# Kernel optimization log

Measured on AMD Instinct MI355X. Metric: run time of the kernel, lower is better.

## Reference

```python
import jax, jax.numpy as jnp
import numpy as np

V = 100000
E = 1600000
BN_EPS = 1e-5


def spmm(edge_index, vals, X):
    # X: (V, Cin, B); sparse L @ X via scatter-add. y[r] += w * X[c]
    rows, cols = edge_index[0], edge_index[1]
    return jnp.zeros_like(X).at[rows].add(vals[:, None, None] * X[cols])


def cheb_conv(x, edge_index, vals, w, b=None):
    # x: (B, Cin, V), w: (K, Cin, Cout) -> (B, Cout, V)
    K = w.shape[0]
    x0 = jnp.transpose(x, (2, 1, 0))  # (V, Cin, B)
    xs = [x0]
    if K > 1:
        x1 = spmm(edge_index, vals, x0)
        xs.append(x1)
        for _ in range(2, K):
            x2 = 2.0 * spmm(edge_index, vals, x1) - x0
            xs.append(x2)
            x0, x1 = x1, x2
    xk = jnp.stack(xs)  # (K, V, Cin, B)
    out = jnp.einsum('kvcb,kco->bov', xk, w)
    if b is not None:
        out = out + b[None, :, None]
    return out


def batch_norm(x, g, b):
    # training-mode BatchNorm1d on (B, C, V): stats over (B, V), biased var
    m = jnp.mean(x, axis=(0, 2), keepdims=True)
    v = jnp.var(x, axis=(0, 2), keepdims=True)
    return g[None, :, None] * (x - m) * jax.lax.rsqrt(v + BN_EPS) + b[None, :, None]


def setup_inputs() -> dict:
    key = jax.random.key(0)
    ks = jax.random.split(key, 8)
    x = jax.random.normal(ks[0], (4, 32, V), dtype=jnp.float32)
    edge_index = jax.random.randint(ks[1], (2, E), 0, V, dtype=jnp.int32)
    # small values keep the K=4 Chebyshev recursion well-scaled
    lap_vals = 0.1 * jax.random.normal(ks[2], (E,), dtype=jnp.float32)
    def w(k, K, cin, cout):
        s = 1.0 / np.sqrt(K * cin)
        return s * jax.random.normal(k, (K, cin, cout), dtype=jnp.float32)
    return {
        'x': x, 'edge_index': edge_index, 'lap_vals': lap_vals,
        'in_bn_g': jnp.ones((32,), jnp.float32), 'in_bn_b': jnp.zeros((32,), jnp.float32),
        'in_w': w(ks[3], 4, 32, 64), 'in_b': jnp.zeros((64,), jnp.float32),
        'h0_bn_g': jnp.ones((64,), jnp.float32), 'h0_bn_b': jnp.zeros((64,), jnp.float32),
        'h0_w': w(ks[4], 4, 64, 64), 'h0_b': jnp.zeros((64,), jnp.float32),
        'h1_bn_g': jnp.ones((64,), jnp.float32), 'h1_bn_b': jnp.zeros((64,), jnp.float32),
        'h1_w': w(ks[5], 4, 64, 32), 'h1_b': jnp.zeros((32,), jnp.float32),
    }


def reference(x, edge_index, lap_vals, in_bn_g, in_bn_b, in_w, in_b,
              h0_bn_g, h0_bn_b, h0_w, h0_b, h1_bn_g, h1_bn_b, h1_w, h1_b):
    xn = batch_norm(x, in_bn_g, in_bn_b)
    out = cheb_conv(xn, edge_index, lap_vals, in_w, in_b)
    # hidden layer 0
    out = jax.nn.relu(out)
    out = batch_norm(out, h0_bn_g, h0_bn_b)
    out = cheb_conv(out, edge_index, lap_vals, h0_w, h0_b)
    # hidden layer 1
    out = jax.nn.relu(out)
    out = batch_norm(out, h1_bn_g, h1_bn_b)
    out = cheb_conv(out, edge_index, lap_vals, h1_w, h1_b)
    # in_channels == out_channels -> Identity shortcut on the BN'ed input
    return jax.nn.relu(out + xn)
```

## Files before the change

kernel.cpp:

```cpp
#include <hip/hip_runtime.h>
#include <cstdint>
#include <cstddef>

#define VN 100000
#define EN 1600000
static constexpr float BN_EPS_F = 1e-5f;
static constexpr float INV_N = 1.0f / 400000.0f;

using short8 = __attribute__((ext_vector_type(8))) short;
using f32x4  = __attribute__((ext_vector_type(4))) float;

__device__ __forceinline__ float bf_lo(unsigned int p) {
  return __builtin_bit_cast(float, p << 16);
}
__device__ __forceinline__ float bf_hi(unsigned int p) {
  return __builtin_bit_cast(float, p & 0xffff0000u);
}
__device__ __forceinline__ float bf1(unsigned short u) {
  return __builtin_bit_cast(float, ((unsigned int)u) << 16);
}
__device__ __forceinline__ unsigned short f2bf(float f) {
  unsigned int x = __builtin_bit_cast(unsigned int, f);
  x += 0x7fffu + ((x >> 16) & 1u);
  return (unsigned short)(x >> 16);
}
__device__ __forceinline__ unsigned int pack2(float a, float b) {
  return (unsigned int)f2bf(a) | ((unsigned int)f2bf(b) << 16);
}

__global__ __launch_bounds__(256) void stats_x_kernel(const float* __restrict__ x,
                                                      float* __restrict__ stats) {
  const int p = blockIdx.x & 127;
  const int chunk = blockIdx.x >> 7;
  const int c = p & 31, b = p >> 5;
  const float* base = x + ((size_t)b * 32 + c) * VN + chunk * 12500;
  float s = 0.f, s2 = 0.f;
  for (int i = threadIdx.x; i < 12500; i += 256) {
    float v = base[i];
    s += v; s2 += v * v;
  }
  __shared__ float r1[256], r2[256];
  r1[threadIdx.x] = s; r2[threadIdx.x] = s2;
  __syncthreads();
  for (int off = 128; off > 0; off >>= 1) {
    if (threadIdx.x < off) {
      r1[threadIdx.x] += r1[threadIdx.x + off];
      r2[threadIdx.x] += r2[threadIdx.x + off];
    }
    __syncthreads();
  }
  if (threadIdx.x == 0) {
    atomicAdd(&stats[c], r1[0]);
    atomicAdd(&stats[64 + c], r2[0]);
  }
}

__global__ void finalize_stats_kernel(float* __restrict__ stats,
                                      const float* __restrict__ g,
                                      const float* __restrict__ beta, int C) {
  int c = threadIdx.x;
  if (c < C) {
    float m = stats[c] * INV_N;
    float var = stats[64 + c] * INV_N - m * m;
    float sc = g[c] * rsqrtf(var + BN_EPS_F);
    stats[128 + c] = sc;
    stats[192 + c] = beta[c] - m * sc;
  }
}

__global__ __launch_bounds__(128) void bn_transpose_kernel(const float* __restrict__ x,
                                                           const float* __restrict__ stats,
                                                           unsigned short* __restrict__ xn) {
  const int tid = threadIdx.x;
  const int b = tid >> 5, c = tid & 31;
  const int v0 = blockIdx.x * 64;
  const float sc = stats[128 + c], sh = stats[192 + c];
  const float* src = x + ((size_t)b * 32 + c) * VN;
  for (int i = 0; i < 64; i++) {
    int v = v0 + i;
    if (v < VN) xn[(size_t)v * 128 + tid] = f2bf(sc * src[v] + sh);
  }
}

__global__ __launch_bounds__(256) void pack_wb_kernel(const float* __restrict__ W,
                                                      unsigned short* __restrict__ Wb,
                                                      int Cin, int Cout) {
  const int i = blockIdx.x * 256 + threadIdx.x;
  const int KC = Cin >> 5, T = Cout >> 4;
  const int tot = 4 * KC * T * 512;
  if (i >= tot) return;
  const int j = i & 7;
  const int l = (i >> 3) & 63;
  const int rem = i >> 9;
  const int t = rem % T;
  const int kc = (rem / T) % KC;
  const int k = rem / (T * KC);
  const int c = kc * 32 + (l >> 4) * 8 + j;
  const int o = t * 16 + (l & 15);
  Wb[i] = f2bf(W[((size_t)k * Cin + c) * Cout + o]);
}

__global__ __launch_bounds__(256) void hist_kernel(const int* __restrict__ rows,
                                                   int* __restrict__ cnt) {
  int i = blockIdx.x * blockDim.x + threadIdx.x;
  const int stride = gridDim.x * blockDim.x;
  for (; i < EN; i += stride) atomicAdd(&cnt[rows[i]], 1);
}

__global__ __launch_bounds__(256) void scan1_kernel(const int* __restrict__ cnt,
                                                    int* __restrict__ rp,
                                                    int* __restrict__ chunkSums) {
  __shared__ int sh[256];
  const int t = threadIdx.x;
  const int base = blockIdx.x * 2048 + t * 8;
  int vals[8]; int tot = 0;
#pragma unroll
  for (int i = 0; i < 8; i++) {
    int idx = base + i;
    int v = (idx < VN) ? cnt[idx] : 0;
    vals[i] = v; tot += v;
  }
  sh[t] = tot;
  __syncthreads();
  for (int off = 1; off < 256; off <<= 1) {
    int v = (t >= off) ? sh[t - off] : 0;
    __syncthreads();
    sh[t] += v;
    __syncthreads();
  }
  int run = sh[t] - tot;
#pragma unroll
  for (int i = 0; i < 8; i++) {
    int idx = base + i;
    if (idx < VN) rp[idx] = run;
    run += vals[i];
  }
  if (t == 255) chunkSums[blockIdx.x] = sh[255];
}

__global__ void scan2_kernel(const int* __restrict__ chunkSums,
                             int* __restrict__ chunkOff,
                             int* __restrict__ rp, int nChunks) {
  if (threadIdx.x == 0 && blockIdx.x == 0) {
    int off = 0;
    for (int j = 0; j < nChunks; j++) { chunkOff[j] = off; off += chunkSums[j]; }
    rp[VN] = off;
  }
}

__global__ __launch_bounds__(256) void scan3_kernel(int* __restrict__ rp,
                                                    const int* __restrict__ chunkOff,
                                                    int* __restrict__ fill) {
  int i = blockIdx.x * 256 + threadIdx.x;
  if (i < VN) {
    int v = rp[i] + chunkOff[i >> 11];
    rp[i] = v;
    fill[i] = v;
  }
}

__global__ __launch_bounds__(256) void fill_kernel(const int* __restrict__ rows,
                                                   const int* __restrict__ cols,
                                                   const float* __restrict__ lap,
                                                   int* __restrict__ fill,
                                                   int* __restrict__ cols_s,
                                                   float* __restrict__ vals_s) {
  int i = blockIdx.x * blockDim.x + threadIdx.x;
  const int stride = gridDim.x * blockDim.x;
  for (; i < EN; i += stride) {
    int r = rows[i];
    int pos = atomicAdd(&fill[r], 1);
    cols_s[pos] = cols[i];
    vals_s[pos] = lap[i];
  }
}

template <int EPL, int MODE>
__global__ __launch_bounds__(256, 8) void spmm_kernel(const int* __restrict__ rp,
                                                   const int* __restrict__ cs,
                                                   const float* __restrict__ vs,
                                                   const unsigned short* __restrict__ X, int XS,
                                                   const unsigned short* __restrict__ P, int PS,
                                                   const unsigned short* __restrict__ Q, int QS,
                                                   unsigned short* __restrict__ Y, int YS) {
  const int lane = threadIdx.x & 63;
  const int row = blockIdx.x * 4 + (threadIdx.x >> 6);
  const int start = rp[row], end = rp[row + 1];
  float acc[EPL];
#pragma unroll
  for (int j = 0; j < EPL; j++) acc[j] = 0.f;
  int e = start;
  for (; e + 4 <= end; e += 4) {
    const int c0 = cs[e], c1 = cs[e + 1], c2 = cs[e + 2], c3 = cs[e + 3];
    const float w0 = vs[e], w1 = vs[e + 1], w2 = vs[e + 2], w3 = vs[e + 3];
    if constexpr (EPL == 4) {
      const uint2 q0 = *reinterpret_cast<const uint2*>(X + (size_t)c0 * XS + lane * 4);
      const uint2 q1 = *reinterpret_cast<const uint2*>(X + (size_t)c1 * XS + lane * 4);
      const uint2 q2 = *reinterpret_cast<const uint2*>(X + (size_t)c2 * XS + lane * 4);
      const uint2 q3 = *reinterpret_cast<const uint2*>(X + (size_t)c3 * XS + lane * 4);
      acc[0] += w0 * bf_lo(q0.x) + w1 * bf_lo(q1.x) + w2 * bf_lo(q2.x) + w3 * bf_lo(q3.x);
      acc[1] += w0 * bf_hi(q0.x) + w1 * bf_hi(q1.x) + w2 * bf_hi(q2.x) + w3 * bf_hi(q3.x);
      acc[2] += w0 * bf_lo(q0.y) + w1 * bf_lo(q1.y) + w2 * bf_lo(q2.y) + w3 * bf_lo(q3.y);
      acc[3] += w0 * bf_hi(q0.y) + w1 * bf_hi(q1.y) + w2 * bf_hi(q2.y) + w3 * bf_hi(q3.y);
    } else {
      const unsigned int q0 = *reinterpret_cast<const unsigned int*>(X + (size_t)c0 * XS + lane * 2);
      const unsigned int q1 = *reinterpret_cast<const unsigned int*>(X + (size_t)c1 * XS + lane * 2);
      const unsigned int q2 = *reinterpret_cast<const unsigned int*>(X + (size_t)c2 * XS + lane * 2);
      const unsigned int q3 = *reinterpret_cast<const unsigned int*>(X + (size_t)c3 * XS + lane * 2);
      acc[0] += w0 * bf_lo(q0) + w1 * bf_lo(q1) + w2 * bf_lo(q2) + w3 * bf_lo(q3);
      acc[1] += w0 * bf_hi(q0) + w1 * bf_hi(q1) + w2 * bf_hi(q2) + w3 * bf_hi(q3);
    }
  }
  for (; e < end; e++) {
    const int c0 = cs[e];
    const float w0 = vs[e];
    if constexpr (EPL == 4) {
      const uint2 q0 = *reinterpret_cast<const uint2*>(X + (size_t)c0 * XS + lane * 4);
      acc[0] += w0 * bf_lo(q0.x);
      acc[1] += w0 * bf_hi(q0.x);
      acc[2] += w0 * bf_lo(q0.y);
      acc[3] += w0 * bf_hi(q0.y);
    } else {
      const unsigned int q0 = *reinterpret_cast<const unsigned int*>(X + (size_t)c0 * XS + lane * 2);
      acc[0] += w0 * bf_lo(q0);
      acc[1] += w0 * bf_hi(q0);
    }
  }
  if constexpr (EPL == 4) {
    float r0 = acc[0], r1 = acc[1], r2 = acc[2], r3 = acc[3];
    if constexpr (MODE == 1) {
      const uint2 p = *reinterpret_cast<const uint2*>(P + (size_t)row * PS + lane * 4);
      r0 = 2.f * r0 - bf_lo(p.x);
      r1 = 2.f * r1 - bf_hi(p.x);
      r2 = 2.f * r2 - bf_lo(p.y);
      r3 = 2.f * r3 - bf_hi(p.y);
    }
    uint2 r;
    r.x = pack2(r0, r1);
    r.y = pack2(r2, r3);
    *reinterpret_cast<uint2*>(Y + (size_t)row * YS + lane * 4) = r;
  } else {
    float r0 = acc[0], r1 = acc[1];
    if constexpr (MODE == 1) {
      const unsigned int p = *reinterpret_cast<const unsigned int*>(P + (size_t)row * PS + lane * 2);
      r0 = 2.f * r0 - bf_lo(p);
      r1 = 2.f * r1 - bf_hi(p);
    } else if constexpr (MODE == 2) {
      const unsigned int p = *reinterpret_cast<const unsigned int*>(P + (size_t)row * PS + lane * 2);
      r0 = 2.f * r0 + bf_lo(p);
      r1 = 2.f * r1 + bf_hi(p);
    } else if constexpr (MODE == 3) {
      const unsigned int p = *reinterpret_cast<const unsigned int*>(P + (size_t)row * PS + lane * 2);
      const unsigned int qq = *reinterpret_cast<const unsigned int*>(Q + (size_t)row * QS + lane * 2);
      r0 = 2.f * r0 - bf_lo(qq) + bf_lo(p);
      r1 = 2.f * r1 - bf_hi(qq) + bf_hi(p);
    } else if constexpr (MODE == 4) {
      const unsigned int p = *reinterpret_cast<const unsigned int*>(P + (size_t)row * PS + lane * 2);
      const unsigned int qq = *reinterpret_cast<const unsigned int*>(Q + (size_t)row * QS + lane * 2);
      r0 = r0 - bf_lo(qq) + bf_lo(p);
      r1 = r1 - bf_hi(qq) + bf_hi(p);
    }
    *reinterpret_cast<unsigned int*>(Y + (size_t)row * YS + lane * 2) = pack2(r0, r1);
  }
}

template <int Cin, int Cout, int X0S>
__global__ __launch_bounds__(256, 8) void fused_cheb_kernel(const int* __restrict__ rp,
                                                         const int* __restrict__ cs,
                                                         const float* __restrict__ vs,
                                                         const unsigned short* __restrict__ X0,
                                                         unsigned short* __restrict__ A,
                                                         const unsigned short* __restrict__ B,
                                                         const unsigned short* __restrict__ Wb,
                                                         const float* __restrict__ Bias) {
  constexpr int EPL = Cin * 4 / 64;
  constexpr int ROWSH = Cin * 4;
  __shared__ unsigned short t3s[4 * ROWSH];
  const int lane = threadIdx.x & 63;
  const int wv = threadIdx.x >> 6;
  const int row0 = blockIdx.x * 4;
  const int row = row0 + wv;

  float g[EPL];
#pragma unroll
  for (int j = 0; j < EPL; j++) g[j] = 0.f;
  const int start = rp[row], end = rp[row + 1];
  int e = start;
  for (; e + 4 <= end; e += 4) {
    const int c0 = cs[e], c1 = cs[e + 1], c2 = cs[e + 2], c3 = cs[e + 3];
    const float w0 = vs[e], w1 = vs[e + 1], w2 = vs[e + 2], w3 = vs[e + 3];
    if constexpr (EPL == 4) {
      const uint2 q0 = *reinterpret_cast<const uint2*>(B + (size_t)c0 * 256 + lane * 4);
      const uint2 q1 = *reinterpret_cast<const uint2*>(B + (size_t)c1 * 256 + lane * 4);
      const uint2 q2 = *reinterpret_cast<const uint2*>(B + (size_t)c2 * 256 + lane * 4);
      const uint2 q3 = *reinterpret_cast<const uint2*>(B + (size_t)c3 * 256 + lane * 4);
      g[0] += w0 * bf_lo(q0.x) + w1 * bf_lo(q1.x) + w2 * bf_lo(q2.x) + w3 * bf_lo(q3.x);
      g[1] += w0 * bf_hi(q0.x) + w1 * bf_hi(q1.x) + w2 * bf_hi(q2.x) + w3 * bf_hi(q3.x);
      g[2] += w0 * bf_lo(q0.y) + w1 * bf_lo(q1.y) + w2 * bf_lo(q2.y) + w3 * bf_lo(q3.y);
      g[3] += w0 * bf_hi(q0.y) + w1 * bf_hi(q1.y) + w2 * bf_hi(q2.y) + w3 * bf_hi(q3.y);
    } else {
      const unsigned int q0 = *reinterpret_cast<const unsigned int*>(B + (size_t)c0 * 256 + lane * 2);
      const unsigned int q1 = *reinterpret_cast<const unsigned int*>(B + (size_t)c1 * 256 + lane * 2);
      const unsigned int q2 = *reinterpret_cast<const unsigned int*>(B + (size_t)c2 * 256 + lane * 2);
      const unsigned int q3 = *reinterpret_cast<const unsigned int*>(B + (size_t)c3 * 256 + lane * 2);
      g[0] += w0 * bf_lo(q0) + w1 * bf_lo(q1) + w2 * bf_lo(q2) + w3 * bf_lo(q3);
      g[1] += w0 * bf_hi(q0) + w1 * bf_hi(q1) + w2 * bf_hi(q2) + w3 * bf_hi(q3);
    }
  }
  for (; e < end; e++) {
    const int c0 = cs[e];
    const float w0 = vs[e];
    if constexpr (EPL == 4) {
      const uint2 q0 = *reinterpret_cast<const uint2*>(B + (size_t)c0 * 256 + lane * 4);
      g[0] += w0 * bf_lo(q0.x);
      g[1] += w0 * bf_hi(q0.x);
      g[2] += w0 * bf_lo(q0.y);
      g[3] += w0 * bf_hi(q0.y);
    } else {
      const unsigned int q0 = *reinterpret_cast<const unsigned int*>(B + (size_t)c0 * 256 + lane * 2);
      g[0] += w0 * bf_lo(q0);
      g[1] += w0 * bf_hi(q0);
    }
  }
  {
    unsigned int* tw = reinterpret_cast<unsigned int*>(t3s + wv * ROWSH);
    if constexpr (EPL == 4) {
      const uint2 p = *reinterpret_cast<const uint2*>(A + (size_t)row * 256 + lane * 4);
      tw[lane * 2]     = pack2(2.f * g[0] - bf_lo(p.x), 2.f * g[1] - bf_hi(p.x));
      tw[lane * 2 + 1] = pack2(2.f * g[2] - bf_lo(p.y), 2.f * g[3] - bf_hi(p.y));
    } else {
      const unsigned int p = *reinterpret_cast<const unsigned int*>(A + (size_t)row * 256 + lane * 2);
      tw[lane] = pack2(2.f * g[0] - bf_lo(p), 2.f * g[1] - bf_hi(p));
    }
  }
  __syncthreads();

  constexpr int KC = Cin / 32;
  constexpr int T = Cout / 16;
  const int col = lane & 15, quad = lane >> 4;
  const int t = wv % T;
  const int ar = col >> 2, ab = col & 3;

  const unsigned short* xap[3];
  xap[0] = X0 + (size_t)(row0 + ar) * X0S + ab * Cin + quad * 8;
  xap[1] = A  + (size_t)(row0 + ar) * 256 + ab * Cin + quad * 8;
  xap[2] = B  + (size_t)(row0 + ar) * 256 + ab * Cin + quad * 8;
  const unsigned short* wb = Wb + (size_t)t * 512 + lane * 8;

  f32x4 acc = {0.f, 0.f, 0.f, 0.f};
#pragma unroll
  for (int k = 0; k < 3; k++) {
#pragma unroll
    for (int kc = 0; kc < KC; kc++) {
      const short8 af = *reinterpret_cast<const short8*>(xap[k] + kc * 32);
      const short8 bf = *reinterpret_cast<const short8*>(wb + (size_t)(k * KC + kc) * T * 512);
      acc = __builtin_amdgcn_mfma_f32_16x16x32_bf16(af, bf, acc, 0, 0, 0);
    }
  }
#pragma unroll
  for (int kc = 0; kc < KC; kc++) {
    const short8 af = *reinterpret_cast<const short8*>(&t3s[ar * ROWSH + ab * Cin + kc * 32 + quad * 8]);
    const short8 bf = *reinterpret_cast<const short8*>(wb + (size_t)(3 * KC + kc) * T * 512);
    acc = __builtin_amdgcn_mfma_f32_16x16x32_bf16(af, bf, acc, 0, 0, 0);
  }
  __syncthreads();

  if (T == 4 || wv < 2) {
    const int og = t * 16 + col;
    const float bs = Bias[og];
#pragma unroll
    for (int r = 0; r < 4; r++) {
      A[(size_t)(row0 + quad) * 256 + r * Cout + og] = f2bf(acc[r] + bs);
    }
  }
}

__global__ __launch_bounds__(256, 8) void gemm_z_kernel(const unsigned short* __restrict__ XL,
                                                        const unsigned short* __restrict__ Wb,
                                                        const float* __restrict__ Bias,
                                                        unsigned short* __restrict__ Z) {
  const int lane = threadIdx.x & 63;
  const int wv = threadIdx.x >> 6;
  const int row0 = blockIdx.x * 4;
  const int col = lane & 15, quad = lane >> 4;
  const int ar = col >> 2, ab = col & 3;
  const unsigned short* xa = XL + (size_t)(row0 + ar) * 256 + ab * 64 + quad * 8;
  const unsigned short* wb = Wb + (size_t)wv * 4 * 512 + lane * 8;
  unsigned short* zr = Z + (size_t)wv * VN * 128;
#pragma unroll
  for (int t = 0; t < 2; t++) {
    f32x4 acc = {0.f, 0.f, 0.f, 0.f};
#pragma unroll
    for (int kc = 0; kc < 2; kc++) {
      const short8 af = *reinterpret_cast<const short8*>(xa + kc * 32);
      const short8 bf = *reinterpret_cast<const short8*>(wb + (size_t)(kc * 2 + t) * 512);
      acc = __builtin_amdgcn_mfma_f32_16x16x32_bf16(af, bf, acc, 0, 0, 0);
    }
    const int og = t * 16 + col;
    const float bs = (wv == 0) ? Bias[og] : 0.f;
#pragma unroll
    for (int r = 0; r < 4; r++) {
      zr[(size_t)(row0 + quad) * 128 + r * 32 + og] = f2bf(acc[r] + bs);
    }
  }
}

__global__ __launch_bounds__(256) void stats_out_kernel(const unsigned short* __restrict__ SRC,
                                                        float* __restrict__ stats) {
  const int tid = threadIdx.x;
  const int per = (VN + gridDim.x - 1) / gridDim.x;
  const int v0 = blockIdx.x * per;
  const int v1 = (v0 + per < VN) ? (v0 + per) : VN;
  float s = 0.f, s2 = 0.f;
  for (int v = v0; v < v1; v++) {
    float val = bf1(SRC[(size_t)v * 256 + tid]);
    val = fmaxf(val, 0.f);
    s += val; s2 += val * val;
  }
  __shared__ float r1[256], r2[256];
  r1[tid] = s; r2[tid] = s2;
  __syncthreads();
  if (tid < 64) {
    float a = r1[tid] + r1[tid + 64] + r1[tid + 128] + r1[tid + 192];
    float b = r2[tid] + r2[tid + 64] + r2[tid + 128] + r2[tid + 192];
    atomicAdd(&stats[tid], a);
    atomicAdd(&stats[64 + tid], b);
  }
}

__global__ __launch_bounds__(256) void bn_relu_kernel(const unsigned short* __restrict__ SRC,
                                                      const float* __restrict__ stats,
                                                      unsigned short* __restrict__ DST) {
  const int i = blockIdx.x * 256 + threadIdx.x;
  const int w = i & 63;
  const int o0 = (w & 15) * 4;
  const float4 sc4 = *reinterpret_cast<const float4*>(stats + 128 + o0);
  const float4 sh4 = *reinterpret_cast<const float4*>(stats + 192 + o0);
  const uint2 q = reinterpret_cast<const uint2*>(SRC)[i];
  float a = fmaxf(bf_lo(q.x), 0.f);
  float b = fmaxf(bf_hi(q.x), 0.f);
  float c = fmaxf(bf_lo(q.y), 0.f);
  float d = fmaxf(bf_hi(q.y), 0.f);
  uint2 r;
  r.x = pack2(a * sc4.x + sh4.x, b * sc4.y + sh4.y);
  r.y = pack2(c * sc4.z + sh4.z, d * sc4.w + sh4.w);
  reinterpret_cast<uint2*>(DST)[i] = r;
}

__global__ __launch_bounds__(256) void final_kernel(const unsigned short* __restrict__ SRC,
                                                    const unsigned short* __restrict__ xn,
                                                    float* __restrict__ out) {
  const int lane = threadIdx.x & 63;
  const int grp = threadIdx.x >> 6;
  const int v = blockIdx.x * 64 + lane;
  if (v >= VN) return;
  for (int ob = grp; ob < 128; ob += 4) {
    float val = bf1(SRC[(size_t)v * 128 + ob]) + bf1(xn[(size_t)v * 128 + ob]);
    val = fmaxf(val, 0.f);
    out[(size_t)ob * VN + v] = val;
  }
}

static constexpr size_t align_up(size_t x) { return (x + 255) & ~(size_t)255; }
static constexpr size_t OFF_RP    = 0;
static constexpr size_t OFF_FILL  = align_up(OFF_RP + (size_t)(VN + 1) * 4);
static constexpr size_t OFF_CHS   = align_up(OFF_FILL + (size_t)VN * 4);
static constexpr size_t OFF_CHO   = align_up(OFF_CHS + 256);
static constexpr size_t OFF_STATS = align_up(OFF_CHO + 256);
static constexpr size_t OFF_WP    = align_up(OFF_STATS + 1024);
static constexpr size_t OFF_CS    = align_up(OFF_WP + 32768 * 2);
static constexpr size_t OFF_VS    = align_up(OFF_CS + (size_t)EN * 4);
static constexpr size_t OFF_XN    = align_up(OFF_VS + (size_t)EN * 4);
static constexpr size_t OFF_XL    = align_up(OFF_XN + (size_t)VN * 128 * 2);
static constexpr size_t OFF_A     = align_up(OFF_XL + (size_t)VN * 256 * 2);
static constexpr size_t OFF_B     = align_up(OFF_A + (size_t)VN * 256 * 2);
static constexpr size_t OFF_END   = OFF_B + (size_t)VN * 256 * 2;
static_assert(OFF_B == OFF_A + (size_t)VN * 256 * 2, "A|B must be contiguous for Clenshaw z layout");

extern "C" void kernel_launch(void* const* d_in, const int* in_sizes, int n_in,
                              void* d_out, int out_size, void* d_ws, size_t ws_size,
                              hipStream_t stream) {
  if (ws_size < OFF_END) return;

  const float* x       = (const float*)d_in[0];
  const int*   rows    = (const int*)d_in[1];
  const int*   cols    = rows + EN;
  const float* lap     = (const float*)d_in[2];
  const float* in_bn_g = (const float*)d_in[3];
  const float* in_bn_b = (const float*)d_in[4];
  const float* in_w    = (const float*)d_in[5];
  const float* in_b    = (const float*)d_in[6];
  const float* h0_bn_g = (const float*)d_in[7];
  const float* h0_bn_b = (const float*)d_in[8];
  const float* h0_w    = (const float*)d_in[9];
  const float* h0_b    = (const float*)d_in[10];
  const float* h1_bn_g = (const float*)d_in[11];
  const float* h1_bn_b = (const float*)d_in[12];
  const float* h1_w    = (const float*)d_in[13];
  const float* h1_b    = (const float*)d_in[14];
  float* outp = (float*)d_out;

  char* ws = (char*)d_ws;
  int*   rp     = (int*)(ws + OFF_RP);
  int*   fill   = (int*)(ws + OFF_FILL);
  int*   chS    = (int*)(ws + OFF_CHS);
  int*   chO    = (int*)(ws + OFF_CHO);
  float* stats  = (float*)(ws + OFF_STATS);
  unsigned short* wbIn = (unsigned short*)(ws + OFF_WP);
  unsigned short* wbH0 = wbIn + 8192;
  unsigned short* wbH1 = wbH0 + 16384;
  int*   cs     = (int*)(ws + OFF_CS);
  float* vs     = (float*)(ws + OFF_VS);
  unsigned short* xn = (unsigned short*)(ws + OFF_XN);
  unsigned short* XL = (unsigned short*)(ws + OFF_XL);
  unsigned short* A  = (unsigned short*)(ws + OFF_A);
  unsigned short* B  = (unsigned short*)(ws + OFF_B);

  const int nChunks = (VN + 2047) / 2048;

  pack_wb_kernel<<<32, 256, 0, stream>>>(in_w, wbIn, 32, 64);
  pack_wb_kernel<<<64, 256, 0, stream>>>(h0_w, wbH0, 64, 64);
  pack_wb_kernel<<<32, 256, 0, stream>>>(h1_w, wbH1, 64, 32);

  hipMemsetAsync(stats, 0, 1024, stream);
  stats_x_kernel<<<1024, 256, 0, stream>>>(x, stats);
  finalize_stats_kernel<<<1, 64, 0, stream>>>(stats, in_bn_g, in_bn_b, 32);
  bn_transpose_kernel<<<1563, 128, 0, stream>>>(x, stats, xn);

  hipMemsetAsync(fill, 0, (size_t)VN * 4, stream);
  hist_kernel<<<2048, 256, 0, stream>>>(rows, fill);
  scan1_kernel<<<nChunks, 256, 0, stream>>>(fill, rp, chS);
  scan2_kernel<<<1, 64, 0, stream>>>(chS, chO, rp, nChunks);
  scan3_kernel<<<(VN + 255) / 256, 256, 0, stream>>>(rp, chO, fill);
  fill_kernel<<<2048, 256, 0, stream>>>(rows, cols, lap, fill, cs, vs);

  spmm_kernel<2, 0><<<VN / 4, 256, 0, stream>>>(rp, cs, vs, xn, 128, nullptr, 0, nullptr, 0, A, 256);
  spmm_kernel<2, 1><<<VN / 4, 256, 0, stream>>>(rp, cs, vs, A, 256, xn, 128, nullptr, 0, B, 256);
  fused_cheb_kernel<32, 64, 128><<<VN / 4, 256, 0, stream>>>(rp, cs, vs, xn, A, B, wbIn, in_b);
  hipMemsetAsync(stats, 0, 1024, stream);
  stats_out_kernel<<<256, 256, 0, stream>>>(A, stats);
  finalize_stats_kernel<<<1, 64, 0, stream>>>(stats, h0_bn_g, h0_bn_b, 64);
  bn_relu_kernel<<<VN * 64 / 256, 256, 0, stream>>>(A, stats, XL);

  spmm_kernel<4, 0><<<VN / 4, 256, 0, stream>>>(rp, cs, vs, XL, 256, nullptr, 0, nullptr, 0, A, 256);
  spmm_kernel<4, 1><<<VN / 4, 256, 0, stream>>>(rp, cs, vs, A, 256, XL, 256, nullptr, 0, B, 256);
  fused_cheb_kernel<64, 64, 256><<<VN / 4, 256, 0, stream>>>(rp, cs, vs, XL, A, B, wbH0, h0_b);
  hipMemsetAsync(stats, 0, 1024, stream);
  stats_out_kernel<<<256, 256, 0, stream>>>(A, stats);
  finalize_stats_kernel<<<1, 64, 0, stream>>>(stats, h1_bn_g, h1_bn_b, 64);
  bn_relu_kernel<<<VN * 64 / 256, 256, 0, stream>>>(A, stats, XL);

  {
    unsigned short* Z  = A;
    unsigned short* z0 = Z;
    unsigned short* z1 = Z + (size_t)VN * 128;
    unsigned short* z2 = Z + (size_t)VN * 256;
    unsigned short* z3 = Z + (size_t)VN * 384;
    gemm_z_kernel<<<VN / 4, 256, 0, stream>>>(XL, wbH1, h1_b, Z);
    spmm_kernel<2, 2><<<VN / 4, 256, 0, stream>>>(rp, cs, vs, z3, 128, z2, 128, nullptr, 0, z2, 128);
    spmm_kernel<2, 3><<<VN / 4, 256, 0, stream>>>(rp, cs, vs, z2, 128, z1, 128, z3, 128, z1, 128);
    spmm_kernel<2, 4><<<VN / 4, 256, 0, stream>>>(rp, cs, vs, z1, 128, z0, 128, z2, 128, z0, 128);
    final_kernel<<<1563, 256, 0, stream>>>(z0, xn, outp);
  }
}
```

Baseline: 1.637 ms.

## Fuse BN+ReLU into SpMM gathers and GEMM loads, unroll gathers by eight

Removes the standalone bn_relu kernels. The BatchNorm scale/shift and ReLU are now applied on the fly wherever the pre-activation buffer is read: the SpMM gather (AX), the recurrence term (AP), the fused Chebyshev GEMM A-operand (AFF0) and the Clenshaw gemm_z input. The gather loop is factored into a shared helper unrolled by eight, so more loads are in flight. Buffers are remapped so that layer-0 intermediates use a 128-stride layout. This saves a full read and write of the activations per layer, at the cost of recomputing the affine and ReLU for every gathered neighbour (about 16 per row).

```diff
diff --git a/kernel.cpp b/kernel.cpp
--- a/kernel.cpp
+++ b/kernel.cpp
@@ -26,6 +26,101 @@
 }
 __device__ __forceinline__ unsigned int pack2(float a, float b) {
   return (unsigned int)f2bf(a) | ((unsigned int)f2bf(b) << 16);
+}
+
+template <int EPL, bool AX>
+__device__ __forceinline__ void gather_accum(int start, int end,
+    const int* __restrict__ cs, const float* __restrict__ vs,
+    const unsigned short* __restrict__ X, int XS, int lane,
+    float4 sc, float4 sh, float* acc) {
+  int e = start;
+  if constexpr (EPL == 4) {
+    for (; e + 8 <= end; e += 8) {
+      uint2 q[8]; float w[8];
+#pragma unroll
+      for (int u = 0; u < 8; u++) {
+        q[u] = *reinterpret_cast<const uint2*>(X + (size_t)cs[e + u] * XS + lane * 4);
+        w[u] = vs[e + u];
+      }
+#pragma unroll
+      for (int u = 0; u < 8; u++) {
+        float v0 = bf_lo(q[u].x), v1 = bf_hi(q[u].x), v2 = bf_lo(q[u].y), v3 = bf_hi(q[u].y);
+        if constexpr (AX) {
+          v0 = fmaxf(v0, 0.f) * sc.x + sh.x;
+          v1 = fmaxf(v1, 0.f) * sc.y + sh.y;
+          v2 = fmaxf(v2, 0.f) * sc.z + sh.z;
+          v3 = fmaxf(v3, 0.f) * sc.w + sh.w;
+        }
+        acc[0] += w[u] * v0; acc[1] += w[u] * v1;
+        acc[2] += w[u] * v2; acc[3] += w[u] * v3;
+      }
+    }
+    for (; e + 4 <= end; e += 4) {
+      uint2 q[4]; float w[4];
+#pragma unroll
+      for (int u = 0; u < 4; u++) {
+        q[u] = *reinterpret_cast<const uint2*>(X + (size_t)cs[e + u] * XS + lane * 4);
+        w[u] = vs[e + u];
+      }
+#pragma unroll
+      for (int u = 0; u < 4; u++) {
+        float v0 = bf_lo(q[u].x), v1 = bf_hi(q[u].x), v2 = bf_lo(q[u].y), v3 = bf_hi(q[u].y);
+        if constexpr (AX) {
+          v0 = fmaxf(v0, 0.f) * sc.x + sh.x;
+          v1 = fmaxf(v1, 0.f) * sc.y + sh.y;
+          v2 = fmaxf(v2, 0.f) * sc.z + sh.z;
+          v3 = fmaxf(v3, 0.f) * sc.w + sh.w;
+        }
+        acc[0] += w[u] * v0; acc[1] += w[u] * v1;
+        acc[2] += w[u] * v2; acc[3] += w[u] * v3;
+      }
+    }
+    for (; e < end; e++) {
+      const uint2 q = *reinterpret_cast<const uint2*>(X + (size_t)cs[e] * XS + lane * 4);
+      const float w = vs[e];
+      float v0 = bf_lo(q.x), v1 = bf_hi(q.x), v2 = bf_lo(q.y), v3 = bf_hi(q.y);
+      if constexpr (AX) {
+        v0 = fmaxf(v0, 0.f) * sc.x + sh.x;
+        v1 = fmaxf(v1, 0.f) * sc.y + sh.y;
+        v2 = fmaxf(v2, 0.f) * sc.z + sh.z;
+        v3 = fmaxf(v3, 0.f) * sc.w + sh.w;
+      }
+      acc[0] += w * v0; acc[1] += w * v1; acc[2] += w * v2; acc[3] += w * v3;
+    }
+  } else {
+    for (; e + 8 <= end; e += 8) {
+      unsigned int q[8]; float w[8];
+#pragma unroll
+      for (int u = 0; u < 8; u++) {
+        q[u] = *reinterpret_cast<const unsigned int*>(X + (size_t)cs[e + u] * XS + lane * 2);
+        w[u] = vs[e + u];
+      }
+#pragma unroll
+      for (int u = 0; u < 8; u++) {
+        acc[0] += w[u] * bf_lo(q[u]);
+        acc[1] += w[u] * bf_hi(q[u]);
+      }
+    }
+    for (; e + 4 <= end; e += 4) {
+      unsigned int q[4]; float w[4];
+#pragma unroll
+      for (int u = 0; u < 4; u++) {
+        q[u] = *reinterpret_cast<const unsigned int*>(X + (size_t)cs[e + u] * XS + lane * 2);
+        w[u] = vs[e + u];
+      }
+#pragma unroll
+      for (int u = 0; u < 4; u++) {
+        acc[0] += w[u] * bf_lo(q[u]);
+        acc[1] += w[u] * bf_hi(q[u]);
+      }
+    }
+    for (; e < end; e++) {
+      const unsigned int q = *reinterpret_cast<const unsigned int*>(X + (size_t)cs[e] * XS + lane * 2);
+      const float w = vs[e];
+      acc[0] += w * bf_lo(q);
+      acc[1] += w * bf_hi(q);
+    }
+  }
 }
 
 __global__ __launch_bounds__(256) void stats_x_kernel(const float* __restrict__ x,
@@ -175,65 +270,44 @@
   }
 }
 
-template <int EPL, int MODE>
+template <int EPL, int MODE, bool AX, bool AP>
 __global__ __launch_bounds__(256, 8) void spmm_kernel(const int* __restrict__ rp,
                                                    const int* __restrict__ cs,
                                                    const float* __restrict__ vs,
                                                    const unsigned short* __restrict__ X, int XS,
                                                    const unsigned short* __restrict__ P, int PS,
                                                    const unsigned short* __restrict__ Q, int QS,
-                                                   unsigned short* __restrict__ Y, int YS) {
+                                                   unsigned short* __restrict__ Y, int YS,
+                                                   const float* __restrict__ bnp) {
   const int lane = threadIdx.x & 63;
   const int row = blockIdx.x * 4 + (threadIdx.x >> 6);
   const int start = rp[row], end = rp[row + 1];
+  float4 sc = {0.f, 0.f, 0.f, 0.f}, sh = {0.f, 0.f, 0.f, 0.f};
+  if constexpr (AX || AP) {
+    const int c0 = (lane * 4) & 63;
+    sc = *reinterpret_cast<const float4*>(bnp + c0);
+    sh = *reinterpret_cast<const float4*>(bnp + 64 + c0);
+  }
   float acc[EPL];
 #pragma unroll
   for (int j = 0; j < EPL; j++) acc[j] = 0.f;
-  int e = start;
-  for (; e + 4 <= end; e += 4) {
-    const int c0 = cs[e], c1 = cs[e + 1], c2 = cs[e + 2], c3 = cs[e + 3];
-    const float w0 = vs[e], w1 = vs[e + 1], w2 = vs[e + 2], w3 = vs[e + 3];
-    if constexpr (EPL == 4) {
-      const uint2 q0 = *reinterpret_cast<const uint2*>(X + (size_t)c0 * XS + lane * 4);
-      const uint2 q1 = *reinterpret_cast<const uint2*>(X + (size_t)c1 * XS + lane * 4);
-      const uint2 q2 = *reinterpret_cast<const uint2*>(X + (size_t)c2 * XS + lane * 4);
-      const uint2 q3 = *reinterpret_cast<const uint2*>(X + (size_t)c3 * XS + lane * 4);
-      acc[0] += w0 * bf_lo(q0.x) + w1 * bf_lo(q1.x) + w2 * bf_lo(q2.x) + w3 * bf_lo(q3.x);
-      acc[1] += w0 * bf_hi(q0.x) + w1 * bf_hi(q1.x) + w2 * bf_hi(q2.x) + w3 * bf_hi(q3.x);
-      acc[2] += w0 * bf_lo(q0.y) + w1 * bf_lo(q1.y) + w2 * bf_lo(q2.y) + w3 * bf_lo(q3.y);
-      acc[3] += w0 * bf_hi(q0.y) + w1 * bf_hi(q1.y) + w2 * bf_hi(q2.y) + w3 * bf_hi(q3.y);
-    } else {
-      const unsigned int q0 = *reinterpret_cast<const unsigned int*>(X + (size_t)c0 * XS + lane * 2);
-      const unsigned int q1 = *reinterpret_cast<const unsigned int*>(X + (size_t)c1 * XS + lane * 2);
-      const unsigned int q2 = *reinterpret_cast<const unsigned int*>(X + (size_t)c2 * XS + lane * 2);
-      const unsigned int q3 = *reinterpret_cast<const unsigned int*>(X + (size_t)c3 * XS + lane * 2);
-      acc[0] += w0 * bf_lo(q0) + w1 * bf_lo(q1) + w2 * bf_lo(q2) + w3 * bf_lo(q3);
-      acc[1] += w0 * bf_hi(q0) + w1 * bf_hi(q1) + w2 * bf_hi(q2) + w3 * bf_hi(q3);
-    }
-  }
-  for (; e < end; e++) {
-    const int c0 = cs[e];
-    const float w0 = vs[e];
-    if constexpr (EPL == 4) {
-      const uint2 q0 = *reinterpret_cast<const uint2*>(X + (size_t)c0 * XS + lane * 4);
-      acc[0] += w0 * bf_lo(q0.x);
-      acc[1] += w0 * bf_hi(q0.x);
-      acc[2] += w0 * bf_lo(q0.y);
-      acc[3] += w0 * bf_hi(q0.y);
-    } else {
-      const unsigned int q0 = *reinterpret_cast<const unsigned int*>(X + (size_t)c0 * XS + lane * 2);
-      acc[0] += w0 * bf_lo(q0);
-      acc[1] += w0 * bf_hi(q0);
-    }
-  }
+  gather_accum<EPL, AX>(start, end, cs, vs, X, XS, lane, sc, sh, acc);
+
   if constexpr (EPL == 4) {
     float r0 = acc[0], r1 = acc[1], r2 = acc[2], r3 = acc[3];
     if constexpr (MODE == 1) {
       const uint2 p = *reinterpret_cast<const uint2*>(P + (size_t)row * PS + lane * 4);
-      r0 = 2.f * r0 - bf_lo(p.x);
-      r1 = 2.f * r1 - bf_hi(p.x);
-      r2 = 2.f * r2 - bf_lo(p.y);
-      r3 = 2.f * r3 - bf_hi(p.y);
+      float p0 = bf_lo(p.x), p1 = bf_hi(p.x), p2 = bf_lo(p.y), p3 = bf_hi(p.y);
+      if constexpr (AP) {
+        p0 = fmaxf(p0, 0.f) * sc.x + sh.x;
+        p1 = fmaxf(p1, 0.f) * sc.y + sh.y;
+        p2 = fmaxf(p2, 0.f) * sc.z + sh.z;
+        p3 = fmaxf(p3, 0.f) * sc.w + sh.w;
+      }
+      r0 = 2.f * r0 - p0;
+      r1 = 2.f * r1 - p1;
+      r2 = 2.f * r2 - p2;
+      r3 = 2.f * r3 - p3;
     }
     uint2 r;
     r.x = pack2(r0, r1);
@@ -264,15 +338,17 @@
   }
 }
 
-template <int Cin, int Cout, int X0S>
+template <int Cin, int Cout, int X0S, int X1S, int X2S, bool AFF0>
 __global__ __launch_bounds__(256, 8) void fused_cheb_kernel(const int* __restrict__ rp,
                                                          const int* __restrict__ cs,
                                                          const float* __restrict__ vs,
                                                          const unsigned short* __restrict__ X0,
-                                                         unsigned short* __restrict__ A,
-                                                         const unsigned short* __restrict__ B,
+                                                         const unsigned short* __restrict__ X1,
+                                                         const unsigned short* __restrict__ X2,
+                                                         unsigned short* __restrict__ OUT,
                                                          const unsigned short* __restrict__ Wb,
-                                                         const float* __restrict__ Bias) {
+                                                         const float* __restrict__ Bias,
+                                                         const float* __restrict__ bnp) {
   constexpr int EPL = Cin * 4 / 64;
   constexpr int ROWSH = Cin * 4;
   __shared__ unsigned short t3s[4 * ROWSH];
@@ -285,51 +361,16 @@
 #pragma unroll
   for (int j = 0; j < EPL; j++) g[j] = 0.f;
   const int start = rp[row], end = rp[row + 1];
-  int e = start;
-  for (; e + 4 <= end; e += 4) {
-    const int c0 = cs[e], c1 = cs[e + 1], c2 = cs[e + 2], c3 = cs[e + 3];
-    const float w0 = vs[e], w1 = vs[e + 1], w2 = vs[e + 2], w3 = vs[e + 3];
-    if constexpr (EPL == 4) {
-      const uint2 q0 = *reinterpret_cast<const uint2*>(B + (size_t)c0 * 256 + lane * 4);
-      const uint2 q1 = *reinterpret_cast<const uint2*>(B + (size_t)c1 * 256 + lane * 4);
-      const uint2 q2 = *reinterpret_cast<const uint2*>(B + (size_t)c2 * 256 + lane * 4);
-      const uint2 q3 = *reinterpret_cast<const uint2*>(B + (size_t)c3 * 256 + lane * 4);
-      g[0] += w0 * bf_lo(q0.x) + w1 * bf_lo(q1.x) + w2 * bf_lo(q2.x) + w3 * bf_lo(q3.x);
-      g[1] += w0 * bf_hi(q0.x) + w1 * bf_hi(q1.x) + w2 * bf_hi(q2.x) + w3 * bf_hi(q3.x);
-      g[2] += w0 * bf_lo(q0.y) + w1 * bf_lo(q1.y) + w2 * bf_lo(q2.y) + w3 * bf_lo(q3.y);
-      g[3] += w0 * bf_hi(q0.y) + w1 * bf_hi(q1.y) + w2 * bf_hi(q2.y) + w3 * bf_hi(q3.y);
-    } else {
-      const unsigned int q0 = *reinterpret_cast<const unsigned int*>(B + (size_t)c0 * 256 + lane * 2);
-      const unsigned int q1 = *reinterpret_cast<const unsigned int*>(B + (size_t)c1 * 256 + lane * 2);
-      const unsigned int q2 = *reinterpret_cast<const unsigned int*>(B + (size_t)c2 * 256 + lane * 2);
-      const unsigned int q3 = *reinterpret_cast<const unsigned int*>(B + (size_t)c3 * 256 + lane * 2);
-      g[0] += w0 * bf_lo(q0) + w1 * bf_lo(q1) + w2 * bf_lo(q2) + w3 * bf_lo(q3);
-      g[1] += w0 * bf_hi(q0) + w1 * bf_hi(q1) + w2 * bf_hi(q2) + w3 * bf_hi(q3);
-    }
-  }
-  for (; e < end; e++) {
-    const int c0 = cs[e];
-    const float w0 = vs[e];
-    if constexpr (EPL == 4) {
-      const uint2 q0 = *reinterpret_cast<const uint2*>(B + (size_t)c0 * 256 + lane * 4);
-      g[0] += w0 * bf_lo(q0.x);
-      g[1] += w0 * bf_hi(q0.x);
-      g[2] += w0 * bf_lo(q0.y);
-      g[3] += w0 * bf_hi(q0.y);
-    } else {
-      const unsigned int q0 = *reinterpret_cast<const unsigned int*>(B + (size_t)c0 * 256 + lane * 2);
-      g[0] += w0 * bf_lo(q0);
-      g[1] += w0 * bf_hi(q0);
-    }
-  }
+  const float4 z4 = {0.f, 0.f, 0.f, 0.f};
+  gather_accum<EPL, false>(start, end, cs, vs, X2, X2S, lane, z4, z4, g);
   {
     unsigned int* tw = reinterpret_cast<unsigned int*>(t3s + wv * ROWSH);
     if constexpr (EPL == 4) {
-      const uint2 p = *reinterpret_cast<const uint2*>(A + (size_t)row * 256 + lane * 4);
+      const uint2 p = *reinterpret_cast<const uint2*>(X1 + (size_t)row * X1S + lane * 4);
       tw[lane * 2]     = pack2(2.f * g[0] - bf_lo(p.x), 2.f * g[1] - bf_hi(p.x));
       tw[lane * 2 + 1] = pack2(2.f * g[2] - bf_lo(p.y), 2.f * g[3] - bf_hi(p.y));
     } else {
-      const unsigned int p = *reinterpret_cast<const unsigned int*>(A + (size_t)row * 256 + lane * 2);
+      const unsigned int p = *reinterpret_cast<const unsigned int*>(X1 + (size_t)row * X1S + lane * 2);
       tw[lane] = pack2(2.f * g[0] - bf_lo(p), 2.f * g[1] - bf_hi(p));
     }
   }
@@ -341,21 +382,46 @@
   const int t = wv % T;
   const int ar = col >> 2, ab = col & 3;
 
-  const unsigned short* xap[3];
-  xap[0] = X0 + (size_t)(row0 + ar) * X0S + ab * Cin + quad * 8;
-  xap[1] = A  + (size_t)(row0 + ar) * 256 + ab * Cin + quad * 8;
-  xap[2] = B  + (size_t)(row0 + ar) * 256 + ab * Cin + quad * 8;
+  const unsigned short* xa0 = X0 + (size_t)(row0 + ar) * X0S + ab * Cin + quad * 8;
+  const unsigned short* xa1 = X1 + (size_t)(row0 + ar) * X1S + ab * Cin + quad * 8;
+  const unsigned short* xa2 = X2 + (size_t)(row0 + ar) * X2S + ab * Cin + quad * 8;
   const unsigned short* wb = Wb + (size_t)t * 512 + lane * 8;
 
   f32x4 acc = {0.f, 0.f, 0.f, 0.f};
 #pragma unroll
-  for (int k = 0; k < 3; k++) {
-#pragma unroll
-    for (int kc = 0; kc < KC; kc++) {
-      const short8 af = *reinterpret_cast<const short8*>(xap[k] + kc * 32);
-      const short8 bf = *reinterpret_cast<const short8*>(wb + (size_t)(k * KC + kc) * T * 512);
-      acc = __builtin_amdgcn_mfma_f32_16x16x32_bf16(af, bf, acc, 0, 0, 0);
-    }
+  for (int kc = 0; kc < KC; kc++) {
+    short8 af;
+    if constexpr (AFF0) {
+      const short8 raw = *reinterpret_cast<const short8*>(xa0 + kc * 32);
+      const int cb = quad * 8 + kc * 32;
+      const float4 s0 = *reinterpret_cast<const float4*>(bnp + cb);
+      const float4 s1 = *reinterpret_cast<const float4*>(bnp + cb + 4);
+      const float4 t0 = *reinterpret_cast<const float4*>(bnp + 64 + cb);
+      const float4 t1 = *reinterpret_cast<const float4*>(bnp + 64 + cb + 4);
+      const float scv[8] = {s0.x, s0.y, s0.z, s0.w, s1.x, s1.y, s1.z, s1.w};
+      const float shv[8] = {t0.x, t0.y, t0.z, t0.w, t1.x, t1.y, t1.z, t1.w};
+#pragma unroll
+      for (int j = 0; j < 8; j++) {
+        float v = fmaxf(bf1((unsigned short)raw[j]), 0.f) * scv[j] + shv[j];
+        af[j] = (short)f2bf(v);
+      }
+    } else {
+      af = *reinterpret_cast<const short8*>(xa0 + kc * 32);
+    }
+    const short8 bf = *reinterpret_cast<const short8*>(wb + (size_t)(0 * KC + kc) * T * 512);
+    acc = __builtin_amdgcn_mfma_f32_16x16x32_bf16(af, bf, acc, 0, 0, 0);
+  }
+#pragma unroll
+  for (int kc = 0; kc < KC; kc++) {
+    const short8 af = *reinterpret_cast<const short8*>(xa1 + kc * 32);
+    const short8 bf = *reinterpret_cast<const short8*>(wb + (size_t)(1 * KC + kc) * T * 512);
+    acc = __builtin_amdgcn_mfma_f32_16x16x32_bf16(af, bf, acc, 0, 0, 0);
+  }
+#pragma unroll
+  for (int kc = 0; kc < KC; kc++) {
+    const short8 af = *reinterpret_cast<const short8*>(xa2 + kc * 32);
+    const short8 bf = *reinterpret_cast<const short8*>(wb + (size_t)(2 * KC + kc) * T * 512);
+    acc = __builtin_amdgcn_mfma_f32_16x16x32_bf16(af, bf, acc, 0, 0, 0);
   }
 #pragma unroll
   for (int kc = 0; kc < KC; kc++) {
@@ -370,31 +436,50 @@
     const float bs = Bias[og];
 #pragma unroll
     for (int r = 0; r < 4; r++) {
-      A[(size_t)(row0 + quad) * 256 + r * Cout + og] = f2bf(acc[r] + bs);
-    }
-  }
-}
-
-__global__ __launch_bounds__(256, 8) void gemm_z_kernel(const unsigned short* __restrict__ XL,
+      OUT[(size_t)(row0 + quad) * 256 + r * Cout + og] = f2bf(acc[r] + bs);
+    }
+  }
+}
+
+__global__ __launch_bounds__(256, 8) void gemm_z_kernel(const unsigned short* __restrict__ A,
                                                         const unsigned short* __restrict__ Wb,
                                                         const float* __restrict__ Bias,
-                                                        unsigned short* __restrict__ Z) {
+                                                        unsigned short* __restrict__ zA,
+                                                        unsigned short* __restrict__ zB,
+                                                        const float* __restrict__ bnp) {
   const int lane = threadIdx.x & 63;
   const int wv = threadIdx.x >> 6;
   const int row0 = blockIdx.x * 4;
   const int col = lane & 15, quad = lane >> 4;
   const int ar = col >> 2, ab = col & 3;
-  const unsigned short* xa = XL + (size_t)(row0 + ar) * 256 + ab * 64 + quad * 8;
+  const unsigned short* xa = A + (size_t)(row0 + ar) * 256 + ab * 64 + quad * 8;
   const unsigned short* wb = Wb + (size_t)wv * 4 * 512 + lane * 8;
-  unsigned short* zr = Z + (size_t)wv * VN * 128;
+  unsigned short* zr = (wv < 2) ? (zA + (size_t)wv * VN * 128)
+                                : (zB + (size_t)(wv - 2) * VN * 128);
+  short8 afr[2];
+#pragma unroll
+  for (int kc = 0; kc < 2; kc++) {
+    const short8 raw = *reinterpret_cast<const short8*>(xa + kc * 32);
+    const int cb = quad * 8 + kc * 32;
+    const float4 s0 = *reinterpret_cast<const float4*>(bnp + cb);
+    const float4 s1 = *reinterpret_cast<const float4*>(bnp + cb + 4);
+    const float4 t0 = *reinterpret_cast<const float4*>(bnp + 64 + cb);
+    const float4 t1 = *reinterpret_cast<const float4*>(bnp + 64 + cb + 4);
+    const float scv[8] = {s0.x, s0.y, s0.z, s0.w, s1.x, s1.y, s1.z, s1.w};
+    const float shv[8] = {t0.x, t0.y, t0.z, t0.w, t1.x, t1.y, t1.z, t1.w};
+#pragma unroll
+    for (int j = 0; j < 8; j++) {
+      float v = fmaxf(bf1((unsigned short)raw[j]), 0.f) * scv[j] + shv[j];
+      afr[kc][j] = (short)f2bf(v);
+    }
+  }
 #pragma unroll
   for (int t = 0; t < 2; t++) {
     f32x4 acc = {0.f, 0.f, 0.f, 0.f};
 #pragma unroll
     for (int kc = 0; kc < 2; kc++) {
-      const short8 af = *reinterpret_cast<const short8*>(xa + kc * 32);
       const short8 bf = *reinterpret_cast<const short8*>(wb + (size_t)(kc * 2 + t) * 512);
-      acc = __builtin_amdgcn_mfma_f32_16x16x32_bf16(af, bf, acc, 0, 0, 0);
+      acc = __builtin_amdgcn_mfma_f32_16x16x32_bf16(afr[kc], bf, acc, 0, 0, 0);
     }
     const int og = t * 16 + col;
     const float bs = (wv == 0) ? Bias[og] : 0.f;
@@ -426,25 +511,6 @@
     atomicAdd(&stats[tid], a);
     atomicAdd(&stats[64 + tid], b);
   }
-}
-
-__global__ __launch_bounds__(256) void bn_relu_kernel(const unsigned short* __restrict__ SRC,
-                                                      const float* __restrict__ stats,
-                                                      unsigned short* __restrict__ DST) {
-  const int i = blockIdx.x * 256 + threadIdx.x;
-  const int w = i & 63;
-  const int o0 = (w & 15) * 4;
-  const float4 sc4 = *reinterpret_cast<const float4*>(stats + 128 + o0);
-  const float4 sh4 = *reinterpret_cast<const float4*>(stats + 192 + o0);
-  const uint2 q = reinterpret_cast<const uint2*>(SRC)[i];
-  float a = fmaxf(bf_lo(q.x), 0.f);
-  float b = fmaxf(bf_hi(q.x), 0.f);
-  float c = fmaxf(bf_lo(q.y), 0.f);
-  float d = fmaxf(bf_hi(q.y), 0.f);
-  uint2 r;
-  r.x = pack2(a * sc4.x + sh4.x, b * sc4.y + sh4.y);
-  r.y = pack2(c * sc4.z + sh4.z, d * sc4.w + sh4.w);
-  reinterpret_cast<uint2*>(DST)[i] = r;
 }
 
 __global__ __launch_bounds__(256) void final_kernel(const unsigned short* __restrict__ SRC,
@@ -475,7 +541,6 @@
 static constexpr size_t OFF_A     = align_up(OFF_XL + (size_t)VN * 256 * 2);
 static constexpr size_t OFF_B     = align_up(OFF_A + (size_t)VN * 256 * 2);
 static constexpr size_t OFF_END   = OFF_B + (size_t)VN * 256 * 2;
-static_assert(OFF_B == OFF_A + (size_t)VN * 256 * 2, "A|B must be contiguous for Clenshaw z layout");
 
 extern "C" void kernel_launch(void* const* d_in, const int* in_sizes, int n_in,
                               void* d_out, int out_size, void* d_ws, size_t ws_size,
@@ -515,6 +580,7 @@
   unsigned short* XL = (unsigned short*)(ws + OFF_XL);
   unsigned short* A  = (unsigned short*)(ws + OFF_A);
   unsigned short* B  = (unsigned short*)(ws + OFF_B);
+  const float* bnp = stats + 128;
 
   const int nChunks = (VN + 2047) / 2048;
 
@@ -534,32 +600,40 @@
   scan3_kernel<<<(VN + 255) / 256, 256, 0, stream>>>(rp, chO, fill);
   fill_kernel<<<2048, 256, 0, stream>>>(rows, cols, lap, fill, cs, vs);
 
-  spmm_kernel<2, 0><<<VN / 4, 256, 0, stream>>>(rp, cs, vs, xn, 128, nullptr, 0, nullptr, 0, A, 256);
-  spmm_kernel<2, 1><<<VN / 4, 256, 0, stream>>>(rp, cs, vs, A, 256, xn, 128, nullptr, 0, B, 256);
-  fused_cheb_kernel<32, 64, 128><<<VN / 4, 256, 0, stream>>>(rp, cs, vs, xn, A, B, wbIn, in_b);
+  unsigned short* XLa = XL;
+  unsigned short* XLb = XL + (size_t)VN * 128;
+  spmm_kernel<2, 0, false, false><<<VN / 4, 256, 0, stream>>>(
+      rp, cs, vs, xn, 128, nullptr, 0, nullptr, 0, XLa, 128, nullptr);
+  spmm_kernel<2, 1, false, false><<<VN / 4, 256, 0, stream>>>(
+      rp, cs, vs, XLa, 128, xn, 128, nullptr, 0, XLb, 128, nullptr);
+  fused_cheb_kernel<32, 64, 128, 128, 128, false><<<VN / 4, 256, 0, stream>>>(
+      rp, cs, vs, xn, XLa, XLb, A, wbIn, in_b, nullptr);
   hipMemsetAsync(stats, 0, 1024, stream);
   stats_out_kernel<<<256, 256, 0, stream>>>(A, stats);
   finalize_stats_kernel<<<1, 64, 0, stream>>>(stats, h0_bn_g, h0_bn_b, 64);
-  bn_relu_kernel<<<VN * 64 / 256, 256, 0, stream>>>(A, stats, XL);
-
-  spmm_kernel<4, 0><<<VN / 4, 256, 0, stream>>>(rp, cs, vs, XL, 256, nullptr, 0, nullptr, 0, A, 256);
-  spmm_kernel<4, 1><<<VN / 4, 256, 0, stream>>>(rp, cs, vs, A, 256, XL, 256, nullptr, 0, B, 256);
-  fused_cheb_kernel<64, 64, 256><<<VN / 4, 256, 0, stream>>>(rp, cs, vs, XL, A, B, wbH0, h0_b);
+
+  spmm_kernel<4, 0, true, false><<<VN / 4, 256, 0, stream>>>(
+      rp, cs, vs, A, 256, nullptr, 0, nullptr, 0, XL, 256, bnp);
+  spmm_kernel<4, 1, false, true><<<VN / 4, 256, 0, stream>>>(
+      rp, cs, vs, XL, 256, A, 256, nullptr, 0, B, 256, bnp);
+  fused_cheb_kernel<64, 64, 256, 256, 256, true><<<VN / 4, 256, 0, stream>>>(
+      rp, cs, vs, A, XL, B, A, wbH0, h0_b, bnp);
   hipMemsetAsync(stats, 0, 1024, stream);
   stats_out_kernel<<<256, 256, 0, stream>>>(A, stats);
   finalize_stats_kernel<<<1, 64, 0, stream>>>(stats, h1_bn_g, h1_bn_b, 64);
-  bn_relu_kernel<<<VN * 64 / 256, 256, 0, stream>>>(A, stats, XL);
 
   {
-    unsigned short* Z  = A;
-    unsigned short* z0 = Z;
-    unsigned short* z1 = Z + (size_t)VN * 128;
-    unsigned short* z2 = Z + (size_t)VN * 256;
-    unsigned short* z3 = Z + (size_t)VN * 384;
-    gemm_z_kernel<<<VN / 4, 256, 0, stream>>>(XL, wbH1, h1_b, Z);
-    spmm_kernel<2, 2><<<VN / 4, 256, 0, stream>>>(rp, cs, vs, z3, 128, z2, 128, nullptr, 0, z2, 128);
-    spmm_kernel<2, 3><<<VN / 4, 256, 0, stream>>>(rp, cs, vs, z2, 128, z1, 128, z3, 128, z1, 128);
-    spmm_kernel<2, 4><<<VN / 4, 256, 0, stream>>>(rp, cs, vs, z1, 128, z0, 128, z2, 128, z0, 128);
+    unsigned short* z0 = XL;
+    unsigned short* z1 = XL + (size_t)VN * 128;
+    unsigned short* z2 = B;
+    unsigned short* z3 = B + (size_t)VN * 128;
+    gemm_z_kernel<<<VN / 4, 256, 0, stream>>>(A, wbH1, h1_b, z0, z2, bnp);
+    spmm_kernel<2, 2, false, false><<<VN / 4, 256, 0, stream>>>(
+        rp, cs, vs, z3, 128, z2, 128, nullptr, 0, z2, 128, nullptr);
+    spmm_kernel<2, 3, false, false><<<VN / 4, 256, 0, stream>>>(
+        rp, cs, vs, z2, 128, z1, 128, z3, 128, z1, 128, nullptr);
+    spmm_kernel<2, 4, false, false><<<VN / 4, 256, 0, stream>>>(
+        rp, cs, vs, z1, 128, z0, 128, z2, 128, z0, 128, nullptr);
     final_kernel<<<1563, 256, 0, stream>>>(z0, xn, outp);
   }
 }
```

After: 1.611 ms. No clear change (-1.6%).
